# Performance work log

Hardware: AMD Instinct MI355X
Metric: run time of the kernel (lower is better)

Reference implementation:

```python
import jax, jax.numpy as jnp
import numpy as np

B, S, C, E = 4, 4096, 256, 256  # batch, seq, in_channel, embedding_dim


def setup_inputs() -> dict:
    key = jax.random.key(0)
    ks = jax.random.split(key, 7)
    scale = 1.0 / np.sqrt(C)
    return {
        "x": jax.random.normal(ks[0], (B, S, C), dtype=jnp.float32),
        "Wq": jax.random.uniform(ks[1], (C, C), jnp.float32, -scale, scale),
        "bq": jax.random.uniform(ks[2], (C,), jnp.float32, -scale, scale),
        "Wk": jax.random.uniform(ks[3], (C, C), jnp.float32, -scale, scale),
        "bk": jax.random.uniform(ks[4], (C,), jnp.float32, -scale, scale),
        "Wv": jax.random.uniform(ks[5], (C, E), jnp.float32, -scale, scale),
        "bv": jax.random.uniform(ks[6], (E,), jnp.float32, -scale, scale),
    }


def reference(x, Wq, bq, Wk, bk, Wv, bv):
    # QKV projections (weights stored as [in, out])
    Q = jnp.einsum("bsc,cd->bsd", x, Wq) + bq  # [B,S,C]
    K = jnp.einsum("bsc,cd->bsd", x, Wk) + bk  # [B,S,C]
    V = jnp.einsum("bsc,ce->bse", x, Wv) + bv  # [B,S,E]
    # Unscaled attention scores, softmax over keys
    scores = jnp.einsum("bqc,bkc->bqk", Q, K)  # [B,S,S]
    attn = jax.nn.softmax(scores, axis=-1)
    attended = jnp.einsum("bqk,bke->bqe", attn, V)  # [B,S,E]
    # Dropout(0.5) treated as identity (eval mode)
    return jax.nn.sigmoid(attended)
```

## Files before the change

kernel.cpp:

```cpp
#include <hip/hip_runtime.h>
#include <cstdint>
#include <cstddef>

#define DI __device__ __forceinline__

typedef __bf16 bf16x8 __attribute__((ext_vector_type(8)));
typedef float f32x4 __attribute__((ext_vector_type(4)));

constexpr int Bb = 4, Ss = 4096, Cc = 256, Ee = 256;

constexpr size_t OFF_QHI = 786432;
constexpr size_t OFF_QLO = 9175040;
constexpr size_t OFF_KHI = 17563648;
constexpr size_t OFF_KLO = 25952256;
constexpr size_t OFF_VHI = 34340864;
constexpr size_t OFF_PML = 42729472;
constexpr size_t OFF_P1  = 42991616;

DI unsigned bf_hi(float f) {
  unsigned u = __builtin_bit_cast(unsigned, f);
  return (u + 0x7fffu + ((u >> 16) & 1u)) >> 16;
}
DI float bf_f(unsigned h) { return __builtin_bit_cast(float, h << 16); }

DI f32x4 mfma16(bf16x8 a, bf16x8 b, f32x4 c) {
  return __builtin_amdgcn_mfma_f32_16x16x32_bf16(a, b, c, 0, 0, 0);
}

DI void gl16(const void* g, void* l) {
  __builtin_amdgcn_global_load_lds(
      (const __attribute__((address_space(1))) unsigned*)g,
      (__attribute__((address_space(3))) unsigned*)l, 16, 0, 0);
}


__global__ __launch_bounds__(256) void k_transpose(
    const float* __restrict__ wq, const float* __restrict__ wk,
    const float* __restrict__ wv, float* __restrict__ wt) {
  const float* src = blockIdx.x == 0 ? wq : (blockIdx.x == 1 ? wk : wv);
  float* dst = wt + (size_t)blockIdx.x * Cc * Cc;
  const int n = threadIdx.x;
  for (int k = 0; k < Cc; k++) dst[n * Cc + k] = src[k * Cc + n];
}

__global__ __launch_bounds__(256, 2) void k_proj(
    const float* __restrict__ x, const float* __restrict__ wt,
    const float* __restrict__ bq, const float* __restrict__ bk,
    const float* __restrict__ bv, char* __restrict__ ws) {
  __shared__ __align__(16) unsigned short xh[64 * 64], xl[64 * 64];
  __shared__ __align__(16) unsigned short wh[64 * 64], wl[64 * 64];
  const int t = threadIdx.x, lane = t & 63, wid = t >> 6;
  const int mat = blockIdx.z;
  const int n0 = blockIdx.y * 64, m0 = blockIdx.x * 64;
  const float* wm = wt + (size_t)mat * Cc * Cc;
  const float* bias = mat == 0 ? bq : (mat == 1 ? bk : bv);

  f32x4 acc[4];
#pragma unroll
  for (int f = 0; f < 4; f++) acc[f] = (f32x4){0.f, 0.f, 0.f, 0.f};

  const int srow = t >> 2, scol = (t & 3) * 16;

  for (int k0 = 0; k0 < Cc; k0 += 64) {
    const float* xs = x + (size_t)(m0 + srow) * Cc + k0 + scol;
    const float* wsrc = wm + (size_t)(n0 + srow) * Cc + k0 + scol;
#pragma unroll
    for (int j = 0; j < 16; j += 4) {
      const int off = srow * 128 + (((scol + j) * 2) ^ ((srow & 7) << 4));
      {
        float4 v = *(const float4*)(xs + j);
        unsigned h0 = bf_hi(v.x), h1 = bf_hi(v.y), h2 = bf_hi(v.z), h3 = bf_hi(v.w);
        unsigned l0 = bf_hi(v.x - bf_f(h0)), l1 = bf_hi(v.y - bf_f(h1));
        unsigned l2 = bf_hi(v.z - bf_f(h2)), l3 = bf_hi(v.w - bf_f(h3));
        *(uint2*)((char*)xh + off) = make_uint2(h0 | (h1 << 16), h2 | (h3 << 16));
        *(uint2*)((char*)xl + off) = make_uint2(l0 | (l1 << 16), l2 | (l3 << 16));
      }
      {
        float4 v = *(const float4*)(wsrc + j);
        unsigned h0 = bf_hi(v.x), h1 = bf_hi(v.y), h2 = bf_hi(v.z), h3 = bf_hi(v.w);
        unsigned l0 = bf_hi(v.x - bf_f(h0)), l1 = bf_hi(v.y - bf_f(h1));
        unsigned l2 = bf_hi(v.z - bf_f(h2)), l3 = bf_hi(v.w - bf_f(h3));
        *(uint2*)((char*)wh + off) = make_uint2(h0 | (h1 << 16), h2 | (h3 << 16));
        *(uint2*)((char*)wl + off) = make_uint2(l0 | (l1 << 16), l2 | (l3 << 16));
      }
    }
    __syncthreads();
#pragma unroll
    for (int c2 = 0; c2 < 2; c2++) {
      const int arow = wid * 16 + (lane & 15);
      const int aby = arow * 128 + ((c2 * 64 + (lane >> 4) * 16) ^ ((arow & 7) << 4));
      bf16x8 ah = *(const bf16x8*)((const char*)xh + aby);
      bf16x8 al = *(const bf16x8*)((const char*)xl + aby);
#pragma unroll
      for (int f = 0; f < 4; f++) {
        const int brow = f * 16 + (lane & 15);
        const int bby = brow * 128 + ((c2 * 64 + (lane >> 4) * 16) ^ ((brow & 7) << 4));
        bf16x8 bh = *(const bf16x8*)((const char*)wh + bby);
        bf16x8 bl = *(const bf16x8*)((const char*)wl + bby);
        acc[f] = mfma16(ah, bh, acc[f]);
        acc[f] = mfma16(al, bh, acc[f]);
        acc[f] = mfma16(ah, bl, acc[f]);
      }
    }
    __syncthreads();
  }

  const int mgbase = m0 + wid * 16 + (lane >> 4) * 4;
#pragma unroll
  for (int f = 0; f < 4; f++) {
    const int ncol = n0 + f * 16 + (lane & 15);
    const float bb = bias[ncol];
    if (mat == 0) {
      unsigned short* qh = (unsigned short*)(ws + OFF_QHI);
      unsigned short* ql = (unsigned short*)(ws + OFF_QLO);
#pragma unroll
      for (int r = 0; r < 4; r++) {
        const int mg = mgbase + r;
        float v = acc[f][r] + bb;
        unsigned h = bf_hi(v);
        qh[(size_t)mg * Cc + ncol] = (unsigned short)h;
        ql[(size_t)mg * Cc + ncol] = (unsigned short)bf_hi(v - bf_f(h));
      }
    } else if (mat == 1) {
      char* kh = ws + OFF_KHI;
      char* kl = ws + OFF_KLO;
#pragma unroll
      for (int r = 0; r < 4; r++) {
        const int mg = mgbase + r;
        const int bidx = mg >> 12, sg = mg & 4095;
        const int kt = sg >> 5, krow = sg & 31;
        const size_t base = ((size_t)(bidx * 128 + kt)) * 16384 +
                            (size_t)(krow * 512 + ((ncol * 2) ^ ((krow & 7) << 4)));
        float v = acc[f][r] + bb;
        unsigned h = bf_hi(v);
        *(unsigned short*)(kh + base) = (unsigned short)h;
        *(unsigned short*)(kl + base) = (unsigned short)bf_hi(v - bf_f(h));
      }
    } else {
      char* vh = ws + OFF_VHI;
      unsigned h[4];
#pragma unroll
      for (int r = 0; r < 4; r++) h[r] = bf_hi(acc[f][r] + bb);
      const int mg = mgbase;
      const int bidx = mg >> 12, sg = mg & 4095;
      const int kt = sg >> 5, kin = sg & 31;
      const int e = ncol;
      const size_t img = (size_t)((e >> 1) * 128 +
                         (((e & 1) * 64 + kin * 2) ^ (((e >> 1) & 7) << 4)));
      *(uint2*)(vh + ((size_t)(bidx * 128 + kt)) * 16384 + img) =
          make_uint2(h[0] | (h[1] << 16), h[2] | (h[3] << 16));
    }
  }
}

__global__ __launch_bounds__(256, 2) void k_attn(
    char* __restrict__ ws, float* __restrict__ out) {
  __shared__ __align__(16) char sbuf[57344];
  const int t = threadIdx.x, lane = t & 63, w = t >> 6;
  const int qt = blockIdx.x, b = blockIdx.y, z = blockIdx.z;
  const int q0 = qt * 64;

  bf16x8 qh_[8], ql_[8];
  {
    const int qrow = q0 + w * 16 + (lane & 15);
    const unsigned short* qph =
        (const unsigned short*)(ws + OFF_QHI) + (size_t)(b * Ss + qrow) * Cc;
    const unsigned short* qpl =
        (const unsigned short*)(ws + OFF_QLO) + (size_t)(b * Ss + qrow) * Cc;
#pragma unroll
    for (int c = 0; c < 8; c++) {
      const int kb = c * 32 + (lane >> 4) * 8;
      qh_[c] = *(const bf16x8*)(qph + kb);
      ql_[c] = *(const bf16x8*)(qpl + kb);
    }
  }

  unsigned srcoff[12];
#pragma unroll
  for (int j = 0; j < 12; j++) {
    const int L = w * 12288 + j * 1024;
    const int r = L >> 14, off = L & 16383;
    const unsigned rb = (r == 0 ? (unsigned)OFF_KHI
                                : (r == 1 ? (unsigned)OFF_KLO : (unsigned)OFF_VHI));
    srcoff[j] = rb + (unsigned)b * 2097152u + (unsigned)z * 1048576u +
                (unsigned)off + (unsigned)(lane * 16);
  }

  f32x4 acc[16];
#pragma unroll
  for (int eg = 0; eg < 16; eg++) acc[eg] = (f32x4){0.f, 0.f, 0.f, 0.f};
  float mrun[4] = {-1e30f, -1e30f, -1e30f, -1e30f};
  float lrun[4] = {0.f, 0.f, 0.f, 0.f};

#pragma unroll
  for (int j = 0; j < 12; j++) gl16(ws + srcoff[j], sbuf + w * 12288 + j * 1024);
  __syncthreads();

  char* const phb = sbuf + 49152 + w * 2048;
  char* const plb = phb + 1024;

  for (int it = 0; it < 64; it++) {
    f32x4 sacc[2];
    sacc[0] = (f32x4){0.f, 0.f, 0.f, 0.f};
    sacc[1] = (f32x4){0.f, 0.f, 0.f, 0.f};
    __builtin_amdgcn_s_setprio(1);
#pragma unroll
    for (int c = 0; c < 8; c++) {
#pragma unroll
      for (int f = 0; f < 2; f++) {
        const int krow = f * 16 + (lane & 15);
        const int kby = krow * 512 + ((c * 64 + (lane >> 4) * 16) ^ ((krow & 7) << 4));
        bf16x8 bh = *(const bf16x8*)(sbuf + kby);
        bf16x8 bl = *(const bf16x8*)(sbuf + 16384 + kby);
        sacc[f] = mfma16(qh_[c], bh, sacc[f]);
        sacc[f] = mfma16(ql_[c], bh, sacc[f]);
        sacc[f] = mfma16(qh_[c], bl, sacc[f]);
      }
    }
    __builtin_amdgcn_s_setprio(0);

    float rmax[4], mnew[4], sc[4], rsum[4];
#pragma unroll
    for (int r = 0; r < 4; r++) rmax[r] = fmaxf(sacc[0][r], sacc[1][r]);
#pragma unroll
    for (int r = 0; r < 4; r++) {
      rmax[r] = fmaxf(rmax[r], __shfl_xor(rmax[r], 1, 64));
      rmax[r] = fmaxf(rmax[r], __shfl_xor(rmax[r], 2, 64));
      rmax[r] = fmaxf(rmax[r], __shfl_xor(rmax[r], 4, 64));
      rmax[r] = fmaxf(rmax[r], __shfl_xor(rmax[r], 8, 64));
      mnew[r] = fmaxf(mrun[r], rmax[r]);
      sc[r] = __expf(mrun[r] - mnew[r]);
      mrun[r] = mnew[r];
      rsum[r] = 0.f;
    }
#pragma unroll
    for (int f = 0; f < 2; f++) {
#pragma unroll
      for (int r = 0; r < 4; r++) {
        float p = __expf(sacc[f][r] - mnew[r]);
        sacc[f][r] = p;
        rsum[r] += p;
      }
    }
#pragma unroll
    for (int r = 0; r < 4; r++) {
      rsum[r] += __shfl_xor(rsum[r], 1, 64);
      rsum[r] += __shfl_xor(rsum[r], 2, 64);
      rsum[r] += __shfl_xor(rsum[r], 4, 64);
      rsum[r] += __shfl_xor(rsum[r], 8, 64);
      lrun[r] = lrun[r] * sc[r] + rsum[r];
    }

#pragma unroll
    for (int f = 0; f < 2; f++) {
#pragma unroll
      for (int r = 0; r < 4; r++) {
        float p = sacc[f][r];
        unsigned hb = bf_hi(p);
        unsigned lb = bf_hi(p - bf_f(hb));
        const int q = (lane >> 4) * 4 + r, kcol = f * 16 + (lane & 15);
        const int off = (q >> 1) * 128 + (((q & 1) * 64 + kcol * 2) ^ (((q >> 1) & 7) << 4));
        *(unsigned short*)(phb + off) = (unsigned short)hb;
        *(unsigned short*)(plb + off) = (unsigned short)lb;
      }
    }

#pragma unroll
    for (int eg = 0; eg < 16; eg++) {
      acc[eg][0] *= sc[0]; acc[eg][1] *= sc[1];
      acc[eg][2] *= sc[2]; acc[eg][3] *= sc[3];
    }

    {
      const int q = lane & 15;
      const int pby = (q >> 1) * 128 +
                      (((q & 1) * 64 + (lane >> 4) * 16) ^ (((q >> 1) & 7) << 4));
      bf16x8 pa_h = *(const bf16x8*)(phb + pby);
      bf16x8 pa_l = *(const bf16x8*)(plb + pby);
      __builtin_amdgcn_s_setprio(1);
#pragma unroll
      for (int eg = 0; eg < 16; eg++) {
        const int erow = eg * 16 + (lane & 15);
        const int vby = (erow >> 1) * 128 +
                        (((erow & 1) * 64 + (lane >> 4) * 16) ^ (((erow >> 1) & 7) << 4));
        bf16x8 bvh = *(const bf16x8*)(sbuf + 32768 + vby);
        acc[eg] = mfma16(pa_h, bvh, acc[eg]);
        acc[eg] = mfma16(pa_l, bvh, acc[eg]);
      }
      __builtin_amdgcn_s_setprio(0);
    }

    __syncthreads();
    if (it < 63) {
#pragma unroll
      for (int j = 0; j < 12; j++) {
        srcoff[j] += 16384;
        gl16(ws + srcoff[j], sbuf + w * 12288 + j * 1024);
      }
    }
    __syncthreads();
  }

  const int qloc0 = w * 16 + (lane >> 4) * 4;
  if (z == 0) {
#pragma unroll
    for (int eg = 0; eg < 16; eg++) {
      const int e = eg * 16 + (lane & 15);
#pragma unroll
      for (int r = 0; r < 4; r++)
        out[((size_t)(b * Ss + q0 + qloc0 + r)) * Ee + e] = acc[eg][r];
    }
  } else {
    unsigned short* p1 = (unsigned short*)(ws + OFF_P1);
#pragma unroll
    for (int eg = 0; eg < 16; eg++) {
      const int e = eg * 16 + (lane & 15);
#pragma unroll
      for (int r = 0; r < 4; r++)
        p1[((size_t)((b * 64 + qt) * 64 + qloc0 + r)) * 256 + e] =
            (unsigned short)bf_hi(acc[eg][r]);
    }
  }
  if ((lane & 15) == 0) {
    float* pml = (float*)(ws + OFF_PML);
#pragma unroll
    for (int r = 0; r < 4; r++) {
      const int q = qloc0 + r;
      pml[(((size_t)(z * 4 + b) * 64 + qt) * 2 + 0) * 64 + q] = mrun[r];
      pml[(((size_t)(z * 4 + b) * 64 + qt) * 2 + 1) * 64 + q] = lrun[r];
    }
  }
}

__global__ __launch_bounds__(256) void k_comb(
    char* __restrict__ ws, float* __restrict__ out) {
  __shared__ float sm0[64], sl0[64], sm1[64], sl1[64];
  const int t = threadIdx.x, qt = blockIdx.x, b = blockIdx.y;
  const float* pml = (const float*)(ws + OFF_PML);
  if (t < 64) {
    sm0[t] = pml[(((size_t)(0 * 4 + b) * 64 + qt) * 2 + 0) * 64 + t];
    sl0[t] = pml[(((size_t)(0 * 4 + b) * 64 + qt) * 2 + 1) * 64 + t];
    sm1[t] = pml[(((size_t)(1 * 4 + b) * 64 + qt) * 2 + 0) * 64 + t];
    sl1[t] = pml[(((size_t)(1 * 4 + b) * 64 + qt) * 2 + 1) * 64 + t];
  }
  __syncthreads();
  const unsigned short* p1 = (const unsigned short*)(ws + OFF_P1);
  for (int q = 0; q < 64; q++) {
    const size_t o = ((size_t)(b * Ss + qt * 64 + q)) * Ee + t;
    float o0 = out[o];
    float o1 = bf_f(p1[((size_t)((b * 64 + qt) * 64 + q)) * 256 + t]);
    float M = fmaxf(sm0[q], sm1[q]);
    float a0 = __expf(sm0[q] - M), a1 = __expf(sm1[q] - M);
    float v = (o0 * a0 + o1 * a1) / (sl0[q] * a0 + sl1[q] * a1);
    out[o] = 1.f / (1.f + __expf(-v));
  }
}

extern "C" void kernel_launch(void* const* d_in, const int* in_sizes, int n_in,
                              void* d_out, int out_size, void* d_ws, size_t ws_size,
                              hipStream_t stream) {
  (void)in_sizes; (void)n_in; (void)out_size; (void)ws_size;
  const float* x  = (const float*)d_in[0];
  const float* Wq = (const float*)d_in[1];
  const float* bq = (const float*)d_in[2];
  const float* Wk = (const float*)d_in[3];
  const float* bk = (const float*)d_in[4];
  const float* Wv = (const float*)d_in[5];
  const float* bv = (const float*)d_in[6];
  float* out = (float*)d_out;
  char* ws = (char*)d_ws;
  float* wt = (float*)ws;

  hipLaunchKernelGGL(k_transpose, dim3(3), dim3(256), 0, stream, Wq, Wk, Wv, wt);
  hipLaunchKernelGGL(k_proj, dim3(256, 4, 3), dim3(256), 0, stream,
                     x, wt, bq, bk, bv, ws);
  hipLaunchKernelGGL(k_attn, dim3(64, Bb, 2), dim3(256), 0, stream, ws, out);
  hipLaunchKernelGGL(k_comb, dim3(64, Bb), dim3(256), 0, stream, ws, out);
}
```

Baseline: 349.8 us.

## Drop P low-part MFMA, lazy softmax rescale, 3-way KV split, packed bf16 converts

Several changes at once. The P·V product now uses a single bf16 P operand instead of a hi/lo split, which halves those MFMAs and the P LDS traffic at some accuracy cost. The online softmax rescales the accumulator only when the tile max exceeds the running max by more than a threshold, skipping the per-tile multiply of 64 accumulators. The KV dimension is split into nz chunks (3 when the workspace is large enough) with occupancy raised to 3 blocks/CU and a generalized combine kernel. Hardware v_cvt_pk_bf16_f32 replaces the manual rounding in the split.

```diff
diff --git a/kernel.cpp b/kernel.cpp
--- a/kernel.cpp
+++ b/kernel.cpp
@@ -15,13 +15,27 @@
 constexpr size_t OFF_KLO = 25952256;
 constexpr size_t OFF_VHI = 34340864;
 constexpr size_t OFF_PML = 42729472;
-constexpr size_t OFF_P1  = 42991616;
 
 DI unsigned bf_hi(float f) {
   unsigned u = __builtin_bit_cast(unsigned, f);
   return (u + 0x7fffu + ((u >> 16) & 1u)) >> 16;
 }
 DI float bf_f(unsigned h) { return __builtin_bit_cast(float, h << 16); }
+
+DI unsigned cvtpk(float a, float b) {
+  unsigned r;
+  asm("v_cvt_pk_bf16_f32 %0, %1, %2" : "=v"(r) : "v"(a), "v"(b));
+  return r;
+}
+DI void split4(float4 v, uint2& h, uint2& l) {
+  unsigned h01 = cvtpk(v.x, v.y), h23 = cvtpk(v.z, v.w);
+  float e0 = __builtin_bit_cast(float, h01 << 16);
+  float e1 = __builtin_bit_cast(float, h01 & 0xffff0000u);
+  float e2 = __builtin_bit_cast(float, h23 << 16);
+  float e3 = __builtin_bit_cast(float, h23 & 0xffff0000u);
+  h = make_uint2(h01, h23);
+  l = make_uint2(cvtpk(v.x - e0, v.y - e1), cvtpk(v.z - e2, v.w - e3));
+}
 
 DI f32x4 mfma16(bf16x8 a, bf16x8 b, f32x4 c) {
   return __builtin_amdgcn_mfma_f32_16x16x32_bf16(a, b, c, 0, 0, 0);
@@ -67,22 +81,13 @@
 #pragma unroll
     for (int j = 0; j < 16; j += 4) {
       const int off = srow * 128 + (((scol + j) * 2) ^ ((srow & 7) << 4));
-      {
-        float4 v = *(const float4*)(xs + j);
-        unsigned h0 = bf_hi(v.x), h1 = bf_hi(v.y), h2 = bf_hi(v.z), h3 = bf_hi(v.w);
-        unsigned l0 = bf_hi(v.x - bf_f(h0)), l1 = bf_hi(v.y - bf_f(h1));
-        unsigned l2 = bf_hi(v.z - bf_f(h2)), l3 = bf_hi(v.w - bf_f(h3));
-        *(uint2*)((char*)xh + off) = make_uint2(h0 | (h1 << 16), h2 | (h3 << 16));
-        *(uint2*)((char*)xl + off) = make_uint2(l0 | (l1 << 16), l2 | (l3 << 16));
-      }
-      {
-        float4 v = *(const float4*)(wsrc + j);
-        unsigned h0 = bf_hi(v.x), h1 = bf_hi(v.y), h2 = bf_hi(v.z), h3 = bf_hi(v.w);
-        unsigned l0 = bf_hi(v.x - bf_f(h0)), l1 = bf_hi(v.y - bf_f(h1));
-        unsigned l2 = bf_hi(v.z - bf_f(h2)), l3 = bf_hi(v.w - bf_f(h3));
-        *(uint2*)((char*)wh + off) = make_uint2(h0 | (h1 << 16), h2 | (h3 << 16));
-        *(uint2*)((char*)wl + off) = make_uint2(l0 | (l1 << 16), l2 | (l3 << 16));
-      }
+      uint2 h, l;
+      split4(*(const float4*)(xs + j), h, l);
+      *(uint2*)((char*)xh + off) = h;
+      *(uint2*)((char*)xl + off) = l;
+      split4(*(const float4*)(wsrc + j), h, l);
+      *(uint2*)((char*)wh + off) = h;
+      *(uint2*)((char*)wl + off) = l;
     }
     __syncthreads();
 #pragma unroll
@@ -153,12 +158,15 @@
   }
 }
 
-__global__ __launch_bounds__(256, 2) void k_attn(
-    char* __restrict__ ws, float* __restrict__ out) {
-  __shared__ __align__(16) char sbuf[57344];
+__global__ __launch_bounds__(256, 3) void k_attn(
+    char* __restrict__ ws, float* __restrict__ out, int nz) {
+  __shared__ __align__(16) char sbuf[53248];
   const int t = threadIdx.x, lane = t & 63, w = t >> 6;
   const int qt = blockIdx.x, b = blockIdx.y, z = blockIdx.z;
   const int q0 = qt * 64;
+  const int ktq = 128 / nz, ktr = 128 % nz;
+  const int kt0 = z * ktq + (z < ktr ? z : ktr);
+  const int cnt = ktq + (z < ktr ? 1 : 0);
 
   bf16x8 qh_[8], ql_[8];
   {
@@ -182,7 +190,7 @@
     const int r = L >> 14, off = L & 16383;
     const unsigned rb = (r == 0 ? (unsigned)OFF_KHI
                                 : (r == 1 ? (unsigned)OFF_KLO : (unsigned)OFF_VHI));
-    srcoff[j] = rb + (unsigned)b * 2097152u + (unsigned)z * 1048576u +
+    srcoff[j] = rb + (unsigned)b * 2097152u + (unsigned)kt0 * 16384u +
                 (unsigned)off + (unsigned)(lane * 16);
   }
 
@@ -196,10 +204,9 @@
   for (int j = 0; j < 12; j++) gl16(ws + srcoff[j], sbuf + w * 12288 + j * 1024);
   __syncthreads();
 
-  char* const phb = sbuf + 49152 + w * 2048;
-  char* const plb = phb + 1024;
-
-  for (int it = 0; it < 64; it++) {
+  char* const phb = sbuf + 49152 + w * 1024;
+
+  for (int it = 0; it < cnt; it++) {
     f32x4 sacc[2];
     sacc[0] = (f32x4){0.f, 0.f, 0.f, 0.f};
     sacc[1] = (f32x4){0.f, 0.f, 0.f, 0.f};
@@ -219,25 +226,40 @@
     }
     __builtin_amdgcn_s_setprio(0);
 
-    float rmax[4], mnew[4], sc[4], rsum[4];
-#pragma unroll
-    for (int r = 0; r < 4; r++) rmax[r] = fmaxf(sacc[0][r], sacc[1][r]);
+    float tm[4];
+#pragma unroll
+    for (int r = 0; r < 4; r++) tm[r] = fmaxf(sacc[0][r], sacc[1][r]);
 #pragma unroll
     for (int r = 0; r < 4; r++) {
-      rmax[r] = fmaxf(rmax[r], __shfl_xor(rmax[r], 1, 64));
-      rmax[r] = fmaxf(rmax[r], __shfl_xor(rmax[r], 2, 64));
-      rmax[r] = fmaxf(rmax[r], __shfl_xor(rmax[r], 4, 64));
-      rmax[r] = fmaxf(rmax[r], __shfl_xor(rmax[r], 8, 64));
-      mnew[r] = fmaxf(mrun[r], rmax[r]);
-      sc[r] = __expf(mrun[r] - mnew[r]);
-      mrun[r] = mnew[r];
-      rsum[r] = 0.f;
-    }
+      tm[r] = fmaxf(tm[r], __shfl_xor(tm[r], 1, 64));
+      tm[r] = fmaxf(tm[r], __shfl_xor(tm[r], 2, 64));
+      tm[r] = fmaxf(tm[r], __shfl_xor(tm[r], 4, 64));
+      tm[r] = fmaxf(tm[r], __shfl_xor(tm[r], 8, 64));
+    }
+    int ok = 1;
+#pragma unroll
+    for (int r = 0; r < 4; r++) ok &= (tm[r] <= mrun[r] + 5.5f) ? 1 : 0;
+    if (!__all(ok)) {
+      float sc[4];
+#pragma unroll
+      for (int r = 0; r < 4; r++) {
+        float mn = fmaxf(mrun[r], tm[r]);
+        sc[r] = __expf(mrun[r] - mn);
+        mrun[r] = mn;
+        lrun[r] *= sc[r];
+      }
+#pragma unroll
+      for (int eg = 0; eg < 16; eg++) {
+        acc[eg][0] *= sc[0]; acc[eg][1] *= sc[1];
+        acc[eg][2] *= sc[2]; acc[eg][3] *= sc[3];
+      }
+    }
+    float rsum[4] = {0.f, 0.f, 0.f, 0.f};
 #pragma unroll
     for (int f = 0; f < 2; f++) {
 #pragma unroll
       for (int r = 0; r < 4; r++) {
-        float p = __expf(sacc[f][r] - mnew[r]);
+        float p = __expf(sacc[f][r] - mrun[r]);
         sacc[f][r] = p;
         rsum[r] += p;
       }
@@ -248,35 +270,25 @@
       rsum[r] += __shfl_xor(rsum[r], 2, 64);
       rsum[r] += __shfl_xor(rsum[r], 4, 64);
       rsum[r] += __shfl_xor(rsum[r], 8, 64);
-      lrun[r] = lrun[r] * sc[r] + rsum[r];
-    }
-
-#pragma unroll
-    for (int f = 0; f < 2; f++) {
-#pragma unroll
-      for (int r = 0; r < 4; r++) {
-        float p = sacc[f][r];
-        unsigned hb = bf_hi(p);
-        unsigned lb = bf_hi(p - bf_f(hb));
-        const int q = (lane >> 4) * 4 + r, kcol = f * 16 + (lane & 15);
-        const int off = (q >> 1) * 128 + (((q & 1) * 64 + kcol * 2) ^ (((q >> 1) & 7) << 4));
-        *(unsigned short*)(phb + off) = (unsigned short)hb;
-        *(unsigned short*)(plb + off) = (unsigned short)lb;
-      }
-    }
-
-#pragma unroll
-    for (int eg = 0; eg < 16; eg++) {
-      acc[eg][0] *= sc[0]; acc[eg][1] *= sc[1];
-      acc[eg][2] *= sc[2]; acc[eg][3] *= sc[3];
+      lrun[r] += rsum[r];
+    }
+
+#pragma unroll
+    for (int r = 0; r < 4; r++) {
+      const unsigned wpk = cvtpk(sacc[0][r], sacc[1][r]);
+      const int q = (lane >> 4) * 4 + r;
+      const int c0 = (lane & 15) * 2;
+      const int lineb = (q >> 1) * 128, sw = ((q >> 1) & 7) << 4, half = (q & 1) * 64;
+      *(unsigned short*)(phb + lineb + ((half + c0) ^ sw)) = (unsigned short)wpk;
+      *(unsigned short*)(phb + lineb + ((half + 32 + c0) ^ sw)) =
+          (unsigned short)(wpk >> 16);
     }
 
     {
       const int q = lane & 15;
       const int pby = (q >> 1) * 128 +
                       (((q & 1) * 64 + (lane >> 4) * 16) ^ (((q >> 1) & 7) << 4));
-      bf16x8 pa_h = *(const bf16x8*)(phb + pby);
-      bf16x8 pa_l = *(const bf16x8*)(plb + pby);
+      bf16x8 pa = *(const bf16x8*)(phb + pby);
       __builtin_amdgcn_s_setprio(1);
 #pragma unroll
       for (int eg = 0; eg < 16; eg++) {
@@ -284,14 +296,13 @@
         const int vby = (erow >> 1) * 128 +
                         (((erow & 1) * 64 + (lane >> 4) * 16) ^ (((erow >> 1) & 7) << 4));
         bf16x8 bvh = *(const bf16x8*)(sbuf + 32768 + vby);
-        acc[eg] = mfma16(pa_h, bvh, acc[eg]);
-        acc[eg] = mfma16(pa_l, bvh, acc[eg]);
+        acc[eg] = mfma16(pa, bvh, acc[eg]);
       }
       __builtin_amdgcn_s_setprio(0);
     }
 
     __syncthreads();
-    if (it < 63) {
+    if (it + 1 < cnt) {
 #pragma unroll
       for (int j = 0; j < 12; j++) {
         srcoff[j] += 16384;
@@ -311,7 +322,8 @@
         out[((size_t)(b * Ss + q0 + qloc0 + r)) * Ee + e] = acc[eg][r];
     }
   } else {
-    unsigned short* p1 = (unsigned short*)(ws + OFF_P1);
+    unsigned short* p1 = (unsigned short*)(ws + OFF_PML + (size_t)nz * 131072 +
+                                           (size_t)(z - 1) * 8388608);
 #pragma unroll
     for (int eg = 0; eg < 16; eg++) {
       const int e = eg * 16 + (lane & 15);
@@ -333,25 +345,33 @@
 }
 
 __global__ __launch_bounds__(256) void k_comb(
-    char* __restrict__ ws, float* __restrict__ out) {
-  __shared__ float sm0[64], sl0[64], sm1[64], sl1[64];
+    char* __restrict__ ws, float* __restrict__ out, int nz) {
+  __shared__ float sm[3][64], sl[3][64];
   const int t = threadIdx.x, qt = blockIdx.x, b = blockIdx.y;
   const float* pml = (const float*)(ws + OFF_PML);
   if (t < 64) {
-    sm0[t] = pml[(((size_t)(0 * 4 + b) * 64 + qt) * 2 + 0) * 64 + t];
-    sl0[t] = pml[(((size_t)(0 * 4 + b) * 64 + qt) * 2 + 1) * 64 + t];
-    sm1[t] = pml[(((size_t)(1 * 4 + b) * 64 + qt) * 2 + 0) * 64 + t];
-    sl1[t] = pml[(((size_t)(1 * 4 + b) * 64 + qt) * 2 + 1) * 64 + t];
+    for (int z = 0; z < nz; z++) {
+      sm[z][t] = pml[(((size_t)(z * 4 + b) * 64 + qt) * 2 + 0) * 64 + t];
+      sl[z][t] = pml[(((size_t)(z * 4 + b) * 64 + qt) * 2 + 1) * 64 + t];
+    }
   }
   __syncthreads();
-  const unsigned short* p1 = (const unsigned short*)(ws + OFF_P1);
+  const unsigned short* p1 =
+      (const unsigned short*)(ws + OFF_PML + (size_t)nz * 131072);
   for (int q = 0; q < 64; q++) {
     const size_t o = ((size_t)(b * Ss + qt * 64 + q)) * Ee + t;
-    float o0 = out[o];
-    float o1 = bf_f(p1[((size_t)((b * 64 + qt) * 64 + q)) * 256 + t]);
-    float M = fmaxf(sm0[q], sm1[q]);
-    float a0 = __expf(sm0[q] - M), a1 = __expf(sm1[q] - M);
-    float v = (o0 * a0 + o1 * a1) / (sl0[q] * a0 + sl1[q] * a1);
+    float M = sm[0][q];
+    for (int z = 1; z < nz; z++) M = fmaxf(M, sm[z][q]);
+    float a0 = __expf(sm[0][q] - M);
+    float num = out[o] * a0, den = sl[0][q] * a0;
+    for (int z = 1; z < nz; z++) {
+      float az = __expf(sm[z][q] - M);
+      float oz = bf_f(p1[(size_t)(z - 1) * 4194304 +
+                         ((size_t)((b * 64 + qt) * 64 + q)) * 256 + t]);
+      num += oz * az;
+      den += sl[z][q] * az;
+    }
+    float v = num / den;
     out[o] = 1.f / (1.f + __expf(-v));
   }
 }
@@ -359,7 +379,7 @@
 extern "C" void kernel_launch(void* const* d_in, const int* in_sizes, int n_in,
                               void* d_out, int out_size, void* d_ws, size_t ws_size,
                               hipStream_t stream) {
-  (void)in_sizes; (void)n_in; (void)out_size; (void)ws_size;
+  (void)in_sizes; (void)n_in; (void)out_size;
   const float* x  = (const float*)d_in[0];
   const float* Wq = (const float*)d_in[1];
   const float* bq = (const float*)d_in[2];
@@ -371,9 +391,11 @@
   char* ws = (char*)d_ws;
   float* wt = (float*)ws;
 
+  const int nz = (ws_size >= 60000000u) ? 3 : 2;
+
   hipLaunchKernelGGL(k_transpose, dim3(3), dim3(256), 0, stream, Wq, Wk, Wv, wt);
   hipLaunchKernelGGL(k_proj, dim3(256, 4, 3), dim3(256), 0, stream,
                      x, wt, bq, bk, bv, ws);
-  hipLaunchKernelGGL(k_attn, dim3(64, Bb, 2), dim3(256), 0, stream, ws, out);
-  hipLaunchKernelGGL(k_comb, dim3(64, Bb), dim3(256), 0, stream, ws, out);
-}
+  hipLaunchKernelGGL(k_attn, dim3(64, Bb, nz), dim3(256), 0, stream, ws, out, nz);
+  hipLaunchKernelGGL(k_comb, dim3(64, Bb), dim3(256), 0, stream, ws, out, nz);
+}
```

After: 553.8 us. +58.3%, slower.
